# Performance work log

Measured on AMD Instinct MI355X. Metric: run time of the kernel, lower is better.

## Reference

```python
import jax, jax.numpy as jnp
import numpy as np
from jax import lax

EPS_DIST = 1e-6   # matches 1/(distances + 1e-6)
EPS_SQRT = 1e-12  # guard sqrt at zero


def setup_inputs() -> dict:
    key = jax.random.key(0)
    kq, ks = jax.random.split(key)
    query = jax.random.normal(kq, (2048, 32, 16), dtype=jnp.float32)
    support = jax.random.normal(ks, (65536, 32, 16), dtype=jnp.float32)
    return {"query": query, "support": support, "k": 16}


def reference(query, support, k):
    # Flatten (N, D, H) -> (N, D*H)
    q = query.reshape(query.shape[0], -1)   # (N_q, F)
    s = support.reshape(support.shape[0], -1)  # (N_s, F)
    # Euclidean distances via ||q||^2 + ||s||^2 - 2 q s^T
    q2 = jnp.sum(q * q, axis=1, keepdims=True)          # (N_q, 1)
    s2 = jnp.sum(s * s, axis=1)                          # (N_s,)
    d2 = q2 + s2[None, :] - 2.0 * (q @ s.T)              # (N_q, N_s)
    dist = jnp.sqrt(jnp.maximum(d2, EPS_SQRT))           # (N_q, N_s)
    # k smallest distances (sorted ascending, like sklearn kneighbors)
    neg_topk, indices = lax.top_k(-dist, k)              # (N_q, k)
    dist_k = -neg_topk
    sim = 1.0 / (dist_k + EPS_DIST)
    weights = sim / jnp.sum(sim, axis=1, keepdims=True)
    return indices, weights.astype(jnp.float32)
```

## Files before the change

### kernel.cpp

```cpp
#include <hip/hip_runtime.h>
#include <math.h>
#include <stdint.h>

#define NQ   2048
#define NS   65536
#define FDIM 512
#define KSEL 16
#define LDA  132
#define LDB  320
#define LDT  132
#define LDTS 129

typedef _Float16 f16x8 __attribute__((ext_vector_type(8)));
typedef _Float16 f16x4 __attribute__((ext_vector_type(4)));
typedef float    f32x16 __attribute__((ext_vector_type(16)));

#define GLL16(dst, src)                                                        \
  __builtin_amdgcn_global_load_lds(                                            \
      (const __attribute__((address_space(1))) void*)(src),                    \
      (__attribute__((address_space(3))) void*)(dst), 16, 0, 0)

__global__ void knn_norms(const float* __restrict__ q, const float* __restrict__ s,
                          float* __restrict__ q2, float* __restrict__ s2) {
  int wid  = (int)blockIdx.x * 4 + ((int)threadIdx.x >> 6);
  int lane = threadIdx.x & 63;
  if (wid >= NQ + NS) return;
  const float* src = (wid < NQ) ? (q + (size_t)wid * FDIM)
                                : (s + (size_t)(wid - NQ) * FDIM);
  float acc = 0.f;
#pragma unroll
  for (int j = 0; j < FDIM / 256; ++j) {
    float4 v = *(const float4*)&src[(lane + 64 * j) * 4];
    acc = fmaf(v.x, v.x, acc); acc = fmaf(v.y, v.y, acc);
    acc = fmaf(v.z, v.z, acc); acc = fmaf(v.w, v.w, acc);
  }
#pragma unroll
  for (int off = 32; off; off >>= 1) acc += __shfl_xor(acc, off, 64);
  if (lane == 0) {
    if (wid < NQ) q2[wid] = acc;
    else          s2[wid - NQ] = acc;
  }
}

__global__ void knn_prep(const float* __restrict__ q, const float* __restrict__ s,
                         float* __restrict__ q2, float* __restrict__ s2,
                         _Float16* __restrict__ qh, _Float16* __restrict__ ql,
                         _Float16* __restrict__ sh, _Float16* __restrict__ slo) {
  int wid  = (int)blockIdx.x * 4 + ((int)threadIdx.x >> 6);
  int lane = threadIdx.x & 63;
  if (wid >= NQ + NS) return;
  const bool isq = wid < NQ;
  const int row  = isq ? wid : wid - NQ;
  const float* src = (isq ? q : s) + (size_t)row * FDIM;
  _Float16* hp = (isq ? qh : sh)  + (size_t)row * FDIM;
  _Float16* lp = (isq ? ql : slo) + (size_t)row * FDIM;
  const float scale = isq ? -2.f : 1.f;
  float acc = 0.f;
#pragma unroll
  for (int j = 0; j < FDIM / 256; ++j) {
    const int e = (lane + 64 * j) * 4;
    float4 v = *(const float4*)&src[e];
    acc = fmaf(v.x, v.x, acc); acc = fmaf(v.y, v.y, acc);
    acc = fmaf(v.z, v.z, acc); acc = fmaf(v.w, v.w, acc);
    f16x4 hv, lv;
    {
      float x0 = v.x * scale; _Float16 h0 = (_Float16)x0;
      float x1 = v.y * scale; _Float16 h1 = (_Float16)x1;
      float x2 = v.z * scale; _Float16 h2 = (_Float16)x2;
      float x3 = v.w * scale; _Float16 h3 = (_Float16)x3;
      hv[0] = h0; lv[0] = (_Float16)(x0 - (float)h0);
      hv[1] = h1; lv[1] = (_Float16)(x1 - (float)h1);
      hv[2] = h2; lv[2] = (_Float16)(x2 - (float)h2);
      hv[3] = h3; lv[3] = (_Float16)(x3 - (float)h3);
    }
    *(f16x4*)&hp[e] = hv;
    *(f16x4*)&lp[e] = lv;
  }
#pragma unroll
  for (int off = 32; off; off >>= 1) acc += __shfl_xor(acc, off, 64);
  if (lane == 0) {
    if (isq) q2[row] = acc;
    else     s2[row] = acc;
  }
}

template <int NCHUNK>
__global__ __launch_bounds__(256, 2) void knn_phase1_mfma(
    const _Float16* __restrict__ qh, const _Float16* __restrict__ ql,
    const _Float16* __restrict__ sh, const _Float16* __restrict__ sl_,
    const float* __restrict__ s2g,
    float* __restrict__ cand_e, int* __restrict__ cand_i) {
  constexpr int CHUNKSZ = NS / NCHUNK;
  constexpr int NST     = CHUNKSZ / 256;

  __shared__ __align__(16) _Float16 Ah[128 * 16];
  __shared__ __align__(16) _Float16 Al[128 * 16];
  __shared__ __align__(16) _Float16 Bh[256 * 16];
  __shared__ __align__(16) _Float16 Bl[256 * 16];
  __shared__ __align__(16) float scrT[64][LDTS];
  __shared__ float s2s[256];

  const int tid = threadIdx.x;
  const int wv  = tid >> 6;
  const int ln  = tid & 63;
  const int lm  = ln & 31;
  const int lh  = ln >> 5;
  const int q0  = (int)blockIdx.x * 128;
  const int chunk = blockIdx.y;

  float ld[KSEL]; int li[KSEL];
#pragma unroll
  for (int s = 0; s < KSEL; ++s) { ld[s] = INFINITY; li[s] = 0x7fffffff; }
  const int srow  = tid >> 1;
  const int shalf = tid & 1;

  const int srcrow  = wv * 32 + (ln >> 1);
  const int srchalf = ln & 1;
  const _Float16* pah = qh + (size_t)(q0 + srcrow) * FDIM + srchalf * 8;
  const _Float16* pal = ql + (size_t)(q0 + srcrow) * FDIM + srchalf * 8;

  _Float16* ldsAh  = Ah + wv * 512;
  _Float16* ldsAl  = Al + wv * 512;
  _Float16* ldsBh0 = Bh + wv * 512;
  _Float16* ldsBh1 = Bh + 2048 + wv * 512;
  _Float16* ldsBl0 = Bl + wv * 512;
  _Float16* ldsBl1 = Bl + 2048 + wv * 512;

  const int aoff = lm * 16 + lh * 8;

#pragma unroll 1
  for (int st = 0; st < NST; ++st) {
    const int s0 = chunk * CHUNKSZ + st * 256;
    s2s[tid] = s2g[s0 + tid];

    const _Float16* pbh = sh  + (size_t)(s0 + srcrow) * FDIM + srchalf * 8;
    const _Float16* pbl = sl_ + (size_t)(s0 + srcrow) * FDIM + srchalf * 8;

    f32x16 acc[4][2];
#pragma unroll
    for (int rt = 0; rt < 4; ++rt)
#pragma unroll
      for (int ct = 0; ct < 2; ++ct)
#pragma unroll
        for (int r = 0; r < 16; ++r) acc[rt][ct][r] = 0.f;

#pragma unroll 1
    for (int kb = 0; kb < FDIM / 16; ++kb) {
      const int ko = kb * 16;
      __syncthreads();
      GLL16(ldsAh,  pah + ko);
      GLL16(ldsAl,  pal + ko);
      GLL16(ldsBh0, pbh + ko);
      GLL16(ldsBh1, pbh + 128 * FDIM + ko);
      GLL16(ldsBl0, pbl + ko);
      GLL16(ldsBl1, pbl + 128 * FDIM + ko);
      asm volatile("s_waitcnt vmcnt(0)" ::: "memory");
      __syncthreads();

      f16x8 bh0 = *(const f16x8*)&Bh[(wv * 64 +  0) * 16 + aoff];
      f16x8 bh1 = *(const f16x8*)&Bh[(wv * 64 + 32) * 16 + aoff];
      f16x8 bl0 = *(const f16x8*)&Bl[(wv * 64 +  0) * 16 + aoff];
      f16x8 bl1 = *(const f16x8*)&Bl[(wv * 64 + 32) * 16 + aoff];
#pragma unroll
      for (int rt = 0; rt < 4; ++rt) {
        f16x8 ahf = *(const f16x8*)&Ah[rt * 512 + aoff];
        f16x8 alf = *(const f16x8*)&Al[rt * 512 + aoff];
        acc[rt][0] = __builtin_amdgcn_mfma_f32_32x32x16_f16(ahf, bh0, acc[rt][0], 0, 0, 0);
        acc[rt][1] = __builtin_amdgcn_mfma_f32_32x32x16_f16(ahf, bh1, acc[rt][1], 0, 0, 0);
        acc[rt][0] = __builtin_amdgcn_mfma_f32_32x32x16_f16(ahf, bl0, acc[rt][0], 0, 0, 0);
        acc[rt][1] = __builtin_amdgcn_mfma_f32_32x32x16_f16(ahf, bl1, acc[rt][1], 0, 0, 0);
        acc[rt][0] = __builtin_amdgcn_mfma_f32_32x32x16_f16(alf, bh0, acc[rt][0], 0, 0, 0);
        acc[rt][1] = __builtin_amdgcn_mfma_f32_32x32x16_f16(alf, bh1, acc[rt][1], 0, 0, 0);
      }
    }

#pragma unroll 1
    for (int sl = 0; sl < 4; ++sl) {
      __syncthreads();
      if (wv == sl) {
#pragma unroll
        for (int ct = 0; ct < 2; ++ct) {
          const int c = ct * 32 + lm;
          const float s2v = s2s[sl * 64 + c];
#pragma unroll
          for (int rt = 0; rt < 4; ++rt) {
#pragma unroll
            for (int r = 0; r < 16; ++r) {
              const int row = rt * 32 + (r & 3) + 8 * (r >> 2) + 4 * lh;
              scrT[c][row] = acc[rt][ct][r] + s2v;
            }
          }
        }
      }
      __syncthreads();
      {
        const int cbase = s0 + sl * 64 + shalf * 32;
        const int coff  = shalf * 32;
        for (int c = 0; c < 32; ++c) {
          const float ev = scrT[coff + c][srow];
          if (ev < ld[KSEL - 1]) {
            bool lt[KSEL];
#pragma unroll
            for (int s = 0; s < KSEL; ++s) lt[s] = ev < ld[s];
            const int iv = cbase + c;
#pragma unroll
            for (int s = KSEL - 1; s >= 1; --s) {
              ld[s] = lt[s - 1] ? ld[s - 1] : (lt[s] ? ev : ld[s]);
              li[s] = lt[s - 1] ? li[s - 1] : (lt[s] ? iv : li[s]);
            }
            if (lt[0]) { ld[0] = ev; li[0] = iv; }
          }
        }
      }
    }
  }

  const size_t base =
      ((size_t)(q0 + srow) * NCHUNK + chunk) * (2 * KSEL) + shalf * KSEL;
#pragma unroll
  for (int j = 0; j < KSEL; ++j) {
    cand_e[base + j] = ld[j];
    cand_i[base + j] = li[j];
  }
}

template <int NCHUNK, int HALVES>
__global__ __launch_bounds__(256, 2) void knn_phase1(
    const float* __restrict__ query, const float* __restrict__ support,
    const float* __restrict__ s2g,
    float* __restrict__ cand_e, int* __restrict__ cand_i) {
  constexpr int CHUNKSZ = NS / NCHUNK;
  constexpr int NST = CHUNKSZ / 256;

  __shared__ __align__(16) float AsT[16][LDA];
  __shared__ __align__(16) float BsT[16 * LDB];
  __shared__ __align__(16) float scrT[64][LDT];
  __shared__ float s2s[256];

  const int tid = threadIdx.x;
  const int tx  = tid & 15;
  const int ty  = tid >> 4;
  const int q0  = (int)blockIdx.x * 128;
  const int chunk = blockIdx.y;

  float ld[KSEL]; int li[KSEL];
#pragma unroll
  for (int s = 0; s < KSEL; ++s) { ld[s] = INFINITY; li[s] = 0x7fffffff; }
  const int  srow  = (HALVES == 2) ? (tid >> 1) : tid;
  const int  shalf = (HALVES == 2) ? (tid & 1) : 0;
  const bool scan_active = (HALVES == 2) || (tid < 128);

  for (int st = 0; st < NST; ++st) {
    const int s0 = chunk * CHUNKSZ + st * 256;
    s2s[tid] = s2g[s0 + tid];

    float acc[8][16];
#pragma unroll
    for (int i = 0; i < 8; ++i)
#pragma unroll
      for (int j = 0; j < 16; ++j) acc[i][j] = 0.f;

    float4 pa[2], pb[4];
    const int rr = tid >> 2, cq = tid & 3, cc = cq << 2;

#pragma unroll
    for (int p = 0; p < 2; ++p)
      pa[p] = *(const float4*)&query[(size_t)(q0 + rr + 64 * p) * FDIM + cc];
#pragma unroll
    for (int p = 0; p < 4; ++p)
      pb[p] = *(const float4*)&support[(size_t)(s0 + rr + 64 * p) * FDIM + cc];

    for (int kb = 0; kb < FDIM / 16; ++kb) {
      __syncthreads();
#pragma unroll
      for (int p = 0; p < 2; ++p) {
        const int r = rr + 64 * p;
        const float v[4] = {pa[p].x, pa[p].y, pa[p].z, pa[p].w};
#pragma unroll
        for (int j = 0; j < 4; ++j) AsT[cq * 4 + j][r] = v[j];
      }
#pragma unroll
      for (int p = 0; p < 4; ++p) {
        const int r  = rr + 64 * p;
        const int pc = 20 * (r >> 4) + (r & 15);
        const float v[4] = {pb[p].x, pb[p].y, pb[p].z, pb[p].w};
#pragma unroll
        for (int j = 0; j < 4; ++j) BsT[(cq * 4 + j) * LDB + pc] = v[j];
      }
      if (kb + 1 < FDIM / 16) {
        const int kc = (kb + 1) * 16 + cc;
#pragma unroll
        for (int p = 0; p < 2; ++p)
          pa[p] = *(const float4*)&query[(size_t)(q0 + rr + 64 * p) * FDIM + kc];
#pragma unroll
        for (int p = 0; p < 4; ++p)
          pb[p] = *(const float4*)&support[(size_t)(s0 + rr + 64 * p) * FDIM + kc];
      }
      __syncthreads();
#pragma unroll 4
      for (int kk = 0; kk < 16; ++kk) {
        float4 a0 = *(const float4*)&AsT[kk][ty * 8];
        float4 a1 = *(const float4*)&AsT[kk][ty * 8 + 4];
        const float* brow = &BsT[kk * LDB + 20 * tx];
        float4 b0 = *(const float4*)&brow[0];
        float4 b1 = *(const float4*)&brow[4];
        float4 b2 = *(const float4*)&brow[8];
        float4 b3 = *(const float4*)&brow[12];
        const float a[8]  = {a0.x, a0.y, a0.z, a0.w, a1.x, a1.y, a1.z, a1.w};
        const float b[16] = {b0.x, b0.y, b0.z, b0.w, b1.x, b1.y, b1.z, b1.w,
                             b2.x, b2.y, b2.z, b2.w, b3.x, b3.y, b3.z, b3.w};
#pragma unroll
        for (int i = 0; i < 8; ++i)
#pragma unroll
          for (int j = 0; j < 16; ++j)
            acc[i][j] = fmaf(a[i], b[j], acc[i][j]);
      }
    }

#pragma unroll 1
    for (int sl = 0; sl < 4; ++sl) {
      __syncthreads();
      if ((tx >> 2) == sl) {
        const int csb = (tx & 3) * 16;
#pragma unroll
        for (int j = 0; j < 16; ++j) {
          const float s2v = s2s[tx * 16 + j];
          float4 v0, v1;
          v0.x = fmaf(-2.f, acc[0][j], s2v);
          v0.y = fmaf(-2.f, acc[1][j], s2v);
          v0.z = fmaf(-2.f, acc[2][j], s2v);
          v0.w = fmaf(-2.f, acc[3][j], s2v);
          v1.x = fmaf(-2.f, acc[4][j], s2v);
          v1.y = fmaf(-2.f, acc[5][j], s2v);
          v1.z = fmaf(-2.f, acc[6][j], s2v);
          v1.w = fmaf(-2.f, acc[7][j], s2v);
          *(float4*)&scrT[csb + j][ty * 8]     = v0;
          *(float4*)&scrT[csb + j][ty * 8 + 4] = v1;
        }
      }
      __syncthreads();
      if (scan_active) {
        const int cbase = s0 + sl * 64 + shalf * 32;
        const int ccount = (HALVES == 2) ? 32 : 64;
        const int coff   = (HALVES == 2) ? shalf * 32 : 0;
        for (int c = 0; c < ccount; ++c) {
          const float ev = scrT[coff + c][srow];
          if (ev < ld[KSEL - 1]) {
            bool lt[KSEL];
#pragma unroll
            for (int s = 0; s < KSEL; ++s) lt[s] = ev < ld[s];
            const int iv = cbase + c;
#pragma unroll
            for (int s = KSEL - 1; s >= 1; --s) {
              ld[s] = lt[s - 1] ? ld[s - 1] : (lt[s] ? ev : ld[s]);
              li[s] = lt[s - 1] ? li[s - 1] : (lt[s] ? iv : li[s]);
            }
            if (lt[0]) { ld[0] = ev; li[0] = iv; }
          }
        }
      }
    }
  }

  if (scan_active) {
    const size_t base =
        ((size_t)(q0 + srow) * NCHUNK + chunk) * (HALVES * KSEL) + shalf * KSEL;
#pragma unroll
    for (int j = 0; j < KSEL; ++j) {
      cand_e[base + j] = ld[j];
      cand_i[base + j] = li[j];
    }
  }
}

template <int NCAND>
__global__ __launch_bounds__(64) void knn_phase2(
    const float* __restrict__ cand_e, const int* __restrict__ cand_i,
    const float* __restrict__ q2g, float* __restrict__ out) {
  constexpr int SLOTS = NCAND / 64;
  __shared__ float wd[KSEL];
  __shared__ int   wi[KSEL];

  const int q    = blockIdx.x;
  const int lane = threadIdx.x;
  const float q2 = q2g[q];
  const float* ce = cand_e + (size_t)q * NCAND;
  const int*   ci = cand_i + (size_t)q * NCAND;

  float d[SLOTS]; int idx[SLOTS];
#pragma unroll
  for (int s = 0; s < SLOTS; ++s) {
    d[s]   = q2 + ce[lane + 64 * s];
    idx[s] = ci[lane + 64 * s];
  }

  for (int r = 0; r < KSEL; ++r) {
    float bd = INFINITY; int bi = 0x7fffffff;
#pragma unroll
    for (int s = 0; s < SLOTS; ++s) {
      bool better = (d[s] < bd) || (d[s] == bd && idx[s] < bi);
      if (better) { bd = d[s]; bi = idx[s]; }
    }
#pragma unroll
    for (int off = 32; off; off >>= 1) {
      float od = __shfl_xor(bd, off, 64);
      int   oi = __shfl_xor(bi, off, 64);
      if (od < bd || (od == bd && oi < bi)) { bd = od; bi = oi; }
    }
#pragma unroll
    for (int s = 0; s < SLOTS; ++s)
      if (idx[s] == bi) { d[s] = INFINITY; idx[s] = 0x7fffffff; }
    if (lane == 0) { wd[r] = bd; wi[r] = bi; }
  }
  __syncthreads();

  float sim = 0.f;
  if (lane < KSEL) {
    const float dist = sqrtf(fmaxf(wd[lane], 1e-12f));
    sim = 1.f / (dist + 1e-6f);
  }
  float tot = sim;
#pragma unroll
  for (int off = 8; off; off >>= 1) tot += __shfl_xor(tot, off, 64);
  if (lane < KSEL) {
    out[(size_t)q * KSEL + lane] = (float)wi[lane];
    out[(size_t)NQ * KSEL + (size_t)q * KSEL + lane] = sim / tot;
  }
}

extern "C" void kernel_launch(void* const* d_in, const int* in_sizes, int n_in,
                              void* d_out, int out_size, void* d_ws, size_t ws_size,
                              hipStream_t stream) {
  const float* query   = (const float*)d_in[0];
  const float* support = (const float*)d_in[1];
  float* out = (float*)d_out;

  float* q2     = (float*)d_ws;
  float* s2     = q2 + NQ;
  float* cand_e = s2 + NS;

  constexpr int NCHUNK = 32;
  const size_t cand_elems = (size_t)NQ * NCHUNK * 2 * KSEL;
  const size_t plane_off  = (size_t)(NQ + NS) + 2 * cand_elems;
  const size_t half_elems = 2 * (size_t)(NQ + NS) * FDIM;
  const size_t need_mfma  = plane_off * 4 + half_elems * 2;
  const size_t need2 = (size_t)(NQ + NS + 2 * NQ * NCHUNK * 2 * KSEL) * 4;

  if (ws_size >= need_mfma) {
    int* cand_i = (int*)(cand_e + cand_elems);
    _Float16* qh  = (_Float16*)((float*)d_ws + plane_off);
    _Float16* ql  = qh + (size_t)NQ * FDIM;
    _Float16* shp = ql + (size_t)NQ * FDIM;
    _Float16* slp = shp + (size_t)NS * FDIM;
    knn_prep<<<(NQ + NS) / 4, 256, 0, stream>>>(query, support, q2, s2,
                                                qh, ql, shp, slp);
    dim3 g1(NQ / 128, NCHUNK);
    knn_phase1_mfma<NCHUNK><<<g1, 256, 0, stream>>>(qh, ql, shp, slp, s2,
                                                    cand_e, cand_i);
    knn_phase2<NCHUNK * 2 * KSEL><<<NQ, 64, 0, stream>>>(cand_e, cand_i, q2, out);
  } else {
    knn_norms<<<(NQ + NS) / 4, 256, 0, stream>>>(query, support, q2, s2);
    if (ws_size >= need2) {
      int* cand_i = (int*)(cand_e + (size_t)NQ * NCHUNK * 2 * KSEL);
      dim3 g1(NQ / 128, NCHUNK);
      knn_phase1<NCHUNK, 2><<<g1, 256, 0, stream>>>(query, support, s2, cand_e, cand_i);
      knn_phase2<NCHUNK * 2 * KSEL><<<NQ, 64, 0, stream>>>(cand_e, cand_i, q2, out);
    } else {
      int* cand_i = (int*)(cand_e + (size_t)NQ * NCHUNK * KSEL);
      dim3 g1(NQ / 128, NCHUNK);
      knn_phase1<NCHUNK, 1><<<g1, 256, 0, stream>>>(query, support, s2, cand_e, cand_i);
      knn_phase2<NCHUNK * KSEL><<<NQ, 64, 0, stream>>>(cand_e, cand_i, q2, out);
    }
  }
}
```

Before: 904.1 us.

## Pre-tile fp16 planes in MFMA fragment order and double-buffer LDS staging

The prep kernel now writes the hi/lo fp16 planes in 32-row, 16-wide k-block tiles laid out in MFMA fragment order, so each staged tile is one contiguous 1 KB block and LDS reads are linear per lane. The GEMM loop double-buffers LDS, issuing the next k-block's global-to-LDS loads before the current block's MFMAs. This drops one of the two barriers per k-step and lets load latency overlap compute. The selection epilogue now uses a smaller 32-column scratch and barriers that skip the vmcnt wait, so in-flight prefetches are not drained; it trades this for twice as many barrier rounds per slice and relies on the prefetch and barrier ordering being correct.

```diff
diff --git a/kernel.cpp b/kernel.cpp
--- a/kernel.cpp
+++ b/kernel.cpp
@@ -9,7 +9,6 @@
 #define LDA  132
 #define LDB  320
 #define LDT  132
-#define LDTS 129
 
 typedef _Float16 f16x8 __attribute__((ext_vector_type(8)));
 typedef _Float16 f16x4 __attribute__((ext_vector_type(4)));
@@ -19,6 +18,8 @@
   __builtin_amdgcn_global_load_lds(                                            \
       (const __attribute__((address_space(1))) void*)(src),                    \
       (__attribute__((address_space(3))) void*)(dst), 16, 0, 0)
+
+#define BAR_NOVM() asm volatile("s_waitcnt lgkmcnt(0)\ns_barrier" ::: "memory")
 
 __global__ void knn_norms(const float* __restrict__ q, const float* __restrict__ s,
                           float* __restrict__ q2, float* __restrict__ s2) {
@@ -46,41 +47,77 @@
                          float* __restrict__ q2, float* __restrict__ s2,
                          _Float16* __restrict__ qh, _Float16* __restrict__ ql,
                          _Float16* __restrict__ sh, _Float16* __restrict__ slo) {
-  int wid  = (int)blockIdx.x * 4 + ((int)threadIdx.x >> 6);
-  int lane = threadIdx.x & 63;
-  if (wid >= NQ + NS) return;
-  const bool isq = wid < NQ;
-  const int row  = isq ? wid : wid - NQ;
-  const float* src = (isq ? q : s) + (size_t)row * FDIM;
-  _Float16* hp = (isq ? qh : sh)  + (size_t)row * FDIM;
-  _Float16* lp = (isq ? ql : slo) + (size_t)row * FDIM;
+  const int wgl = (int)blockIdx.x * 4 + ((int)threadIdx.x >> 6);
+  const int ln  = threadIdx.x & 63;
+  const int lm  = ln & 31;
+  const int lh  = ln >> 5;
+  constexpr int NRBQ = NQ / 32;
+  constexpr int NRB  = (NQ + NS) / 32;
+  if (wgl >= NRB) return;
+  const bool isq = wgl < NRBQ;
+  const int rb = isq ? wgl : wgl - NRBQ;
+  const float* src = (isq ? q : s) + ((size_t)rb * 32 + lm) * FDIM + lh * 8;
+  _Float16* hp = (isq ? qh : sh)  + (size_t)rb * (32 * FDIM);
+  _Float16* lp = (isq ? ql : slo) + (size_t)rb * (32 * FDIM);
   const float scale = isq ? -2.f : 1.f;
   float acc = 0.f;
-#pragma unroll
-  for (int j = 0; j < FDIM / 256; ++j) {
-    const int e = (lane + 64 * j) * 4;
-    float4 v = *(const float4*)&src[e];
-    acc = fmaf(v.x, v.x, acc); acc = fmaf(v.y, v.y, acc);
-    acc = fmaf(v.z, v.z, acc); acc = fmaf(v.w, v.w, acc);
-    f16x4 hv, lv;
-    {
-      float x0 = v.x * scale; _Float16 h0 = (_Float16)x0;
-      float x1 = v.y * scale; _Float16 h1 = (_Float16)x1;
-      float x2 = v.z * scale; _Float16 h2 = (_Float16)x2;
-      float x3 = v.w * scale; _Float16 h3 = (_Float16)x3;
-      hv[0] = h0; lv[0] = (_Float16)(x0 - (float)h0);
-      hv[1] = h1; lv[1] = (_Float16)(x1 - (float)h1);
-      hv[2] = h2; lv[2] = (_Float16)(x2 - (float)h2);
-      hv[3] = h3; lv[3] = (_Float16)(x3 - (float)h3);
-    }
-    *(f16x4*)&hp[e] = hv;
-    *(f16x4*)&lp[e] = lv;
-  }
-#pragma unroll
-  for (int off = 32; off; off >>= 1) acc += __shfl_xor(acc, off, 64);
-  if (lane == 0) {
-    if (isq) q2[row] = acc;
-    else     s2[row] = acc;
+#pragma unroll 4
+  for (int kb = 0; kb < FDIM / 16; ++kb) {
+    float4 v0 = *(const float4*)&src[kb * 16];
+    float4 v1 = *(const float4*)&src[kb * 16 + 4];
+    const float x[8] = {v0.x, v0.y, v0.z, v0.w, v1.x, v1.y, v1.z, v1.w};
+    f16x8 hv, lv;
+#pragma unroll
+    for (int j = 0; j < 8; ++j) {
+      acc = fmaf(x[j], x[j], acc);
+      float xs = x[j] * scale;
+      _Float16 h = (_Float16)xs;
+      hv[j] = h;
+      lv[j] = (_Float16)(xs - (float)h);
+    }
+    *(f16x8*)&hp[(size_t)kb * 512 + ln * 8] = hv;
+    *(f16x8*)&lp[(size_t)kb * 512 + ln * 8] = lv;
+  }
+  acc += __shfl_xor(acc, 32, 64);
+  if (ln < 32) {
+    if (isq) q2[rb * 32 + lm] = acc;
+    else     s2[rb * 32 + lm] = acc;
+  }
+}
+
+template <int CT>
+__device__ __forceinline__ void sel_slice(
+    const f32x16 (&acc)[4][2], float (&ld)[KSEL], int (&li)[KSEL],
+    float (*scr)[129], const float* s2s,
+    int wv, int lm, int lh, int srow, int shalf, int s0, int slpair) {
+  BAR_NOVM();
+  if (wv == slpair) {
+    const int c = lm;
+    const float s2v = s2s[slpair * 64 + CT * 32 + c];
+#pragma unroll
+    for (int rt = 0; rt < 4; ++rt)
+#pragma unroll
+      for (int r = 0; r < 16; ++r) {
+        const int row = rt * 32 + (r & 3) + 8 * (r >> 2) + 4 * lh;
+        scr[c][row] = acc[rt][CT][r] + s2v;
+      }
+  }
+  BAR_NOVM();
+  const int cbase = s0 + slpair * 64 + CT * 32 + shalf * 16;
+  for (int c = 0; c < 16; ++c) {
+    const float ev = scr[shalf * 16 + c][srow];
+    if (ev < ld[KSEL - 1]) {
+      bool lt[KSEL];
+#pragma unroll
+      for (int s = 0; s < KSEL; ++s) lt[s] = ev < ld[s];
+      const int iv = cbase + c;
+#pragma unroll
+      for (int s = KSEL - 1; s >= 1; --s) {
+        ld[s] = lt[s - 1] ? ld[s - 1] : (lt[s] ? ev : ld[s]);
+        li[s] = lt[s - 1] ? li[s - 1] : (lt[s] ? iv : li[s]);
+      }
+      if (lt[0]) { ld[0] = ev; li[0] = iv; }
+    }
   }
 }
 
@@ -92,12 +129,10 @@
     float* __restrict__ cand_e, int* __restrict__ cand_i) {
   constexpr int CHUNKSZ = NS / NCHUNK;
   constexpr int NST     = CHUNKSZ / 256;
-
-  __shared__ __align__(16) _Float16 Ah[128 * 16];
-  __shared__ __align__(16) _Float16 Al[128 * 16];
-  __shared__ __align__(16) _Float16 Bh[256 * 16];
-  __shared__ __align__(16) _Float16 Bl[256 * 16];
-  __shared__ __align__(16) float scrT[64][LDTS];
+  constexpr int BUFH    = 12288;
+
+  __shared__ __align__(16) _Float16 stg[2 * BUFH];
+  __shared__ __align__(16) float scr[32][129];
   __shared__ float s2s[256];
 
   const int tid = threadIdx.x;
@@ -107,6 +142,7 @@
   const int lh  = ln >> 5;
   const int q0  = (int)blockIdx.x * 128;
   const int chunk = blockIdx.y;
+  const int rbA = q0 >> 5;
 
   float ld[KSEL]; int li[KSEL];
 #pragma unroll
@@ -114,27 +150,23 @@
   const int srow  = tid >> 1;
   const int shalf = tid & 1;
 
-  const int srcrow  = wv * 32 + (ln >> 1);
-  const int srchalf = ln & 1;
-  const _Float16* pah = qh + (size_t)(q0 + srcrow) * FDIM + srchalf * 8;
-  const _Float16* pal = ql + (size_t)(q0 + srcrow) * FDIM + srchalf * 8;
-
-  _Float16* ldsAh  = Ah + wv * 512;
-  _Float16* ldsAl  = Al + wv * 512;
-  _Float16* ldsBh0 = Bh + wv * 512;
-  _Float16* ldsBh1 = Bh + 2048 + wv * 512;
-  _Float16* ldsBl0 = Bl + wv * 512;
-  _Float16* ldsBl1 = Bl + 2048 + wv * 512;
-
-  const int aoff = lm * 16 + lh * 8;
+  auto STAGE = [&](int buf, int st_, int kb_) {
+    const int s0r = (chunk * CHUNKSZ + st_ * 256) >> 5;
+    _Float16* d = stg + buf * BUFH;
+    const size_t lo = (size_t)ln * 8;
+    GLL16(d +        wv * 512, qh  + ((size_t)(rbA + wv)     * 32 + kb_) * 512 + lo);
+    GLL16(d + 2048 + wv * 512, ql  + ((size_t)(rbA + wv)     * 32 + kb_) * 512 + lo);
+    GLL16(d + 4096 + wv * 512,       sh  + ((size_t)(s0r + wv)     * 32 + kb_) * 512 + lo);
+    GLL16(d + 4096 + (wv + 4) * 512, sh  + ((size_t)(s0r + wv + 4) * 32 + kb_) * 512 + lo);
+    GLL16(d + 8192 + wv * 512,       sl_ + ((size_t)(s0r + wv)     * 32 + kb_) * 512 + lo);
+    GLL16(d + 8192 + (wv + 4) * 512, sl_ + ((size_t)(s0r + wv + 4) * 32 + kb_) * 512 + lo);
+  };
 
 #pragma unroll 1
   for (int st = 0; st < NST; ++st) {
     const int s0 = chunk * CHUNKSZ + st * 256;
     s2s[tid] = s2g[s0 + tid];
-
-    const _Float16* pbh = sh  + (size_t)(s0 + srcrow) * FDIM + srchalf * 8;
-    const _Float16* pbl = sl_ + (size_t)(s0 + srcrow) * FDIM + srchalf * 8;
+    if (st == 0) STAGE(0, 0, 0);
 
     f32x16 acc[4][2];
 #pragma unroll
@@ -144,27 +176,23 @@
 #pragma unroll
         for (int r = 0; r < 16; ++r) acc[rt][ct][r] = 0.f;
 
-#pragma unroll 1
+    __syncthreads();
+
+#pragma unroll 2
     for (int kb = 0; kb < FDIM / 16; ++kb) {
-      const int ko = kb * 16;
-      __syncthreads();
-      GLL16(ldsAh,  pah + ko);
-      GLL16(ldsAl,  pal + ko);
-      GLL16(ldsBh0, pbh + ko);
-      GLL16(ldsBh1, pbh + 128 * FDIM + ko);
-      GLL16(ldsBl0, pbl + ko);
-      GLL16(ldsBl1, pbl + 128 * FDIM + ko);
-      asm volatile("s_waitcnt vmcnt(0)" ::: "memory");
-      __syncthreads();
-
-      f16x8 bh0 = *(const f16x8*)&Bh[(wv * 64 +  0) * 16 + aoff];
-      f16x8 bh1 = *(const f16x8*)&Bh[(wv * 64 + 32) * 16 + aoff];
-      f16x8 bl0 = *(const f16x8*)&Bl[(wv * 64 +  0) * 16 + aoff];
-      f16x8 bl1 = *(const f16x8*)&Bl[(wv * 64 + 32) * 16 + aoff];
+      if (kb < FDIM / 16 - 1)      STAGE((kb + 1) & 1, st, kb + 1);
+      else if (st + 1 < NST)       STAGE(0, st + 1, 0);
+
+      const _Float16* base = stg + (kb & 1) * BUFH;
+      const int lo8 = ln * 8;
+      f16x8 bh0 = *(const f16x8*)&base[4096 + (wv * 2 + 0) * 512 + lo8];
+      f16x8 bh1 = *(const f16x8*)&base[4096 + (wv * 2 + 1) * 512 + lo8];
+      f16x8 bl0 = *(const f16x8*)&base[8192 + (wv * 2 + 0) * 512 + lo8];
+      f16x8 bl1 = *(const f16x8*)&base[8192 + (wv * 2 + 1) * 512 + lo8];
 #pragma unroll
       for (int rt = 0; rt < 4; ++rt) {
-        f16x8 ahf = *(const f16x8*)&Ah[rt * 512 + aoff];
-        f16x8 alf = *(const f16x8*)&Al[rt * 512 + aoff];
+        f16x8 ahf = *(const f16x8*)&base[       rt * 512 + lo8];
+        f16x8 alf = *(const f16x8*)&base[2048 + rt * 512 + lo8];
         acc[rt][0] = __builtin_amdgcn_mfma_f32_32x32x16_f16(ahf, bh0, acc[rt][0], 0, 0, 0);
         acc[rt][1] = __builtin_amdgcn_mfma_f32_32x32x16_f16(ahf, bh1, acc[rt][1], 0, 0, 0);
         acc[rt][0] = __builtin_amdgcn_mfma_f32_32x32x16_f16(ahf, bl0, acc[rt][0], 0, 0, 0);
@@ -172,46 +200,13 @@
         acc[rt][0] = __builtin_amdgcn_mfma_f32_32x32x16_f16(alf, bh0, acc[rt][0], 0, 0, 0);
         acc[rt][1] = __builtin_amdgcn_mfma_f32_32x32x16_f16(alf, bh1, acc[rt][1], 0, 0, 0);
       }
+      if (kb < FDIM / 16 - 1) __syncthreads();
     }
 
 #pragma unroll 1
-    for (int sl = 0; sl < 4; ++sl) {
-      __syncthreads();
-      if (wv == sl) {
-#pragma unroll
-        for (int ct = 0; ct < 2; ++ct) {
-          const int c = ct * 32 + lm;
-          const float s2v = s2s[sl * 64 + c];
-#pragma unroll
-          for (int rt = 0; rt < 4; ++rt) {
-#pragma unroll
-            for (int r = 0; r < 16; ++r) {
-              const int row = rt * 32 + (r & 3) + 8 * (r >> 2) + 4 * lh;
-              scrT[c][row] = acc[rt][ct][r] + s2v;
-            }
-          }
-        }
-      }
-      __syncthreads();
-      {
-        const int cbase = s0 + sl * 64 + shalf * 32;
-        const int coff  = shalf * 32;
-        for (int c = 0; c < 32; ++c) {
-          const float ev = scrT[coff + c][srow];
-          if (ev < ld[KSEL - 1]) {
-            bool lt[KSEL];
-#pragma unroll
-            for (int s = 0; s < KSEL; ++s) lt[s] = ev < ld[s];
-            const int iv = cbase + c;
-#pragma unroll
-            for (int s = KSEL - 1; s >= 1; --s) {
-              ld[s] = lt[s - 1] ? ld[s - 1] : (lt[s] ? ev : ld[s]);
-              li[s] = lt[s - 1] ? li[s - 1] : (lt[s] ? iv : li[s]);
-            }
-            if (lt[0]) { ld[0] = ev; li[0] = iv; }
-          }
-        }
-      }
+    for (int slpair = 0; slpair < 4; ++slpair) {
+      sel_slice<0>(acc, ld, li, scr, s2s, wv, lm, lh, srow, shalf, s0, slpair);
+      sel_slice<1>(acc, ld, li, scr, s2s, wv, lm, lh, srow, shalf, s0, slpair);
     }
   }
 
@@ -452,8 +447,8 @@
     _Float16* ql  = qh + (size_t)NQ * FDIM;
     _Float16* shp = ql + (size_t)NQ * FDIM;
     _Float16* slp = shp + (size_t)NS * FDIM;
-    knn_prep<<<(NQ + NS) / 4, 256, 0, stream>>>(query, support, q2, s2,
-                                                qh, ql, shp, slp);
+    knn_prep<<<(NQ + NS) / (32 * 4), 256, 0, stream>>>(query, support, q2, s2,
+                                                       qh, ql, shp, slp);
     dim3 g1(NQ / 128, NCHUNK);
     knn_phase1_mfma<NCHUNK><<<g1, 256, 0, stream>>>(qh, ql, shp, slp, s2,
                                                     cand_e, cand_i);
```

Measured after the change: 828.0 us. 8.4% less time.
